# Performance work log

Hardware: AMD Instinct MI355X
Metric: run time of the kernel (lower is better)

The kernel has to match this reference:

```python
import jax, jax.numpy as jnp
import numpy as np

B, T, C, HS = 8, 4096, 1024, 128

def setup_inputs() -> dict:
    key = jax.random.key(0)
    kx, kq, kk, kv = jax.random.split(key, 4)
    x = jax.random.normal(kx, (B, T, C), dtype=jnp.float32)
    # Linear weights stored as [in, out] so projection is x @ W
    Wq = jax.random.normal(kq, (C, HS), dtype=jnp.float32) * (C ** -0.5)
    Wk = jax.random.normal(kk, (C, HS), dtype=jnp.float32) * (C ** -0.5)
    Wv = jax.random.normal(kv, (C, HS), dtype=jnp.float32) * (C ** -0.5)
    return {"x": x, "Wq": Wq, "Wk": Wk, "Wv": Wv}

def reference(x, Wq, Wk, Wv):
    # one head of causal self-attention (dropout=0.0 -> identity)
    q = x @ Wq  # [B,T,HS]
    k = x @ Wk
    v = x @ Wv
    scale = q.shape[-1] ** -0.5
    scores = jnp.einsum('bqd,bkd->bqk', q, k) * scale  # [B,T,T]
    t = q.shape[1]
    causal = jnp.tril(jnp.ones((t, t), dtype=bool))
    scores = jnp.where(causal, scores, jnp.finfo(scores.dtype).min)
    weights = jax.nn.softmax(scores, axis=-1)
    out = jnp.einsum('bqk,bkd->bqd', weights, v)  # [B,T,HS]
    return out
```

## Files before the change

kernel.cpp:

```cpp
#include <hip/hip_runtime.h>
#include <hip/hip_bf16.h>

#define TB 8
#define TT 4096
#define TC 1024
#define THS 128

typedef __bf16 bf16;
typedef __attribute__((ext_vector_type(8))) __bf16 bf16x8;
typedef __attribute__((ext_vector_type(2))) __bf16 bf16x2;
typedef __attribute__((ext_vector_type(4))) float f32x4;
typedef __attribute__((ext_vector_type(16))) float f32x16;

__device__ __forceinline__ unsigned pkbf(float a, float b) {
    bf16x2 t = { (bf16)a, (bf16)b };
    return __builtin_bit_cast(unsigned, t);
}

__device__ __forceinline__ void gload16(const void* g, void* l) {
    __builtin_amdgcn_global_load_lds(
        (const __attribute__((address_space(1))) void*)g,
        (__attribute__((address_space(3))) void*)l, 16, 0, 0);
}

__global__ __launch_bounds__(256) void wt_kernel(const float* __restrict__ Wq,
                                                 const float* __restrict__ Wk,
                                                 const float* __restrict__ Wv,
                                                 bf16* __restrict__ Wt) {
    __shared__ float tile[64][65];
    const int tid = threadIdx.x;
    const int idx = blockIdx.x;
    const int w = idx >> 5;
    const int kt = (idx & 31) >> 1, ntb = idx & 1;
    const int k0 = kt * 64, n0 = ntb * 64;
    const float* W = (w == 0) ? Wq : (w == 1) ? Wk : Wv;
    #pragma unroll
    for (int i = 0; i < 4; i++) {
        int r = (tid >> 4) + i * 16;
        int c4 = (tid & 15) * 4;
        float4 x4 = *reinterpret_cast<const float4*>(&W[(long)(k0 + r) * 128 + n0 + c4]);
        tile[r][c4 + 0] = x4.x; tile[r][c4 + 1] = x4.y;
        tile[r][c4 + 2] = x4.z; tile[r][c4 + 3] = x4.w;
    }
    __syncthreads();
    const int n = tid >> 2, kk = (tid & 3) * 16;
    bf16 o[16];
    #pragma unroll
    for (int j = 0; j < 16; j++) o[j] = (bf16)tile[kk + j][n];
    bf16* dst = &Wt[(long)((w << 7) + n0 + n) * 1024 + k0 + kk];
    *reinterpret_cast<bf16x8*>(dst)     = *reinterpret_cast<bf16x8*>(&o[0]);
    *reinterpret_cast<bf16x8*>(dst + 8) = *reinterpret_cast<bf16x8*>(&o[8]);
}

__global__ __launch_bounds__(256, 2) void qkv_kernel(const float* __restrict__ x,
                                                     const bf16* __restrict__ Wt,
                                                     bf16* __restrict__ Q,
                                                     bf16* __restrict__ K,
                                                     bf16* __restrict__ V) {
    __shared__ __align__(1024) char wsm[2][24576];
    __shared__ __align__(1024) char xsm[2][8192];
    const int tid = threadIdx.x;
    const int wave = tid >> 6, lane = tid & 63;
    const int lr = lane & 15, g = lane >> 4;
    const long row0 = (long)blockIdx.x * 64;

    long wOff[6]; int wLoff[6];
    #pragma unroll
    for (int i = 0; i < 6; i++) {
        int D = i * 4096 + wave * 1024 + lane * 16;
        int n = D >> 6, kb2 = D & 63;
        wOff[i] = (long)n * 2048 + (kb2 ^ ((n & 3) << 4));
        wLoff[i] = i * 4096 + wave * 1024;
    }
    long xOff[2]; int xLoff[2];
    #pragma unroll
    for (int i = 0; i < 2; i++) {
        int D = wave * 2048 + i * 1024 + lane * 16;
        int xr = D >> 7, xcb = D & 127;
        xOff[i] = (long)xr * 4096 + (xcb ^ ((xr & 7) << 4));
        xLoff[i] = wave * 2048 + i * 1024;
    }
    const char* xb = (const char*)x + row0 * 4096;
    const char* wb = (const char*)Wt;

    f32x4 acc[4][6] = {};

    {
        #pragma unroll
        for (int i = 0; i < 6; i++) gload16(wb + wOff[i], &wsm[0][0] + wLoff[i]);
        #pragma unroll
        for (int i = 0; i < 2; i++) gload16(xb + xOff[i], &xsm[0][0] + xLoff[i]);
    }
    asm volatile("s_waitcnt vmcnt(0)" ::: "memory");
    __builtin_amdgcn_s_barrier();

    const int asw = (lr & 7) << 4;
    const int bsw = (lr & 3) << 4;
    #pragma unroll 1
    for (int s = 0; s < 32; s++) {
        const int bi = s & 1;
        if (s + 1 < 32) {
            const char* wsrc = wb + (long)(s + 1) * 64;
            const char* xsrc = xb + (long)(s + 1) * 128;
            #pragma unroll
            for (int i = 0; i < 6; i++) gload16(wsrc + wOff[i], &wsm[bi ^ 1][0] + wLoff[i]);
            #pragma unroll
            for (int i = 0; i < 2; i++) gload16(xsrc + xOff[i], &xsm[bi ^ 1][0] + xLoff[i]);
        }
        const char* xp = &xsm[bi][0];
        const char* wp = &wsm[bi][0];
        bf16x8 a[4];
        #pragma unroll
        for (int ar = 0; ar < 4; ar++) {
            const int rbase = (ar * 16 + lr) * 128;
            f32x4 lo = *reinterpret_cast<const f32x4*>(xp + rbase + ((g * 32) ^ asw));
            f32x4 hi4 = *reinterpret_cast<const f32x4*>(xp + rbase + ((g * 32 + 16) ^ asw));
            uint4 u;
            u.x = pkbf(lo[0], lo[1]); u.y = pkbf(lo[2], lo[3]);
            u.z = pkbf(hi4[0], hi4[1]); u.w = pkbf(hi4[2], hi4[3]);
            a[ar] = __builtin_bit_cast(bf16x8, u);
        }
        #pragma unroll
        for (int nt = 0; nt < 6; nt++) {
            const int n = wave * 96 + nt * 16 + lr;
            bf16x8 bfr = *reinterpret_cast<const bf16x8*>(wp + n * 64 + ((g * 16) ^ bsw));
            #pragma unroll
            for (int ar = 0; ar < 4; ar++)
                acc[ar][nt] = __builtin_amdgcn_mfma_f32_16x16x32_bf16(a[ar], bfr, acc[ar][nt], 0, 0, 0);
        }
        asm volatile("s_waitcnt vmcnt(0)" ::: "memory");
        __builtin_amdgcn_s_barrier();
    }
    const float qscale = 0.08838834764831845f;
    bf16* outs[3] = {Q, K, V};
    #pragma unroll
    for (int nt = 0; nt < 6; nt++) {
        const int col = wave * 96 + nt * 16 + lr;
        const int w = col >> 7, d = col & 127;
        #pragma unroll
        for (int ar = 0; ar < 4; ar++)
            #pragma unroll
            for (int r = 0; r < 4; r++) {
                float val = acc[ar][nt][r];
                if (w == 0) val *= qscale;
                long row = row0 + ar * 16 + g * 4 + r;
                outs[w][row * 128 + d] = (bf16)val;
            }
    }
}

__global__ __launch_bounds__(256) void vtrans_kernel(const bf16* __restrict__ V,
                                                     bf16* __restrict__ Vtt) {
    __shared__ __align__(16) bf16 tile[64][136];
    const int tid = threadIdx.x;
    const int b = blockIdx.y;
    const int tt = blockIdx.x;
    const long ibase = ((long)b * TT + tt * 64) * 128;
    #pragma unroll
    for (int i = 0; i < 4; i++) {
        int slot = tid + 256 * i;
        int r = slot >> 4, c8 = (slot & 15) * 8;
        *reinterpret_cast<bf16x8*>(&tile[r][c8]) =
            *reinterpret_cast<const bf16x8*>(&V[ibase + r * 128 + c8]);
    }
    __syncthreads();
    #pragma unroll
    for (int i = 0; i < 4; i++) {
        int slot = tid + 256 * i;
        int d = slot >> 3, t8 = (slot & 7) * 8;
        bf16x8 v;
        #pragma unroll
        for (int j = 0; j < 8; j++) v[j] = tile[t8 + j][d];
        *reinterpret_cast<bf16x8*>(&Vtt[(((long)b * 64 + tt) * 128 + d) * 64 + t8]) = v;
    }
}

__global__ __launch_bounds__(512, 2) void attn_kernel(const bf16* __restrict__ Q,
                                                      const bf16* __restrict__ K,
                                                      const bf16* __restrict__ Vtt,
                                                      float* __restrict__ out) {
    __shared__ __align__(1024) char smem[131072];
    __shared__ float mlb[6 * 64];
    const int tid = threadIdx.x;
    const int wave = tid >> 6, lane = tid & 63;
    const int c = lane & 31, hi = lane >> 5;
    const int qs = wave >> 2, kvq = wave & 3;
    const int kswz = ((c & 7) << 4) ^ (((c >> 3) & 1) << 7);
    const int vswz = (c & 7) << 4;
    const int v = blockIdx.x >> 3, b = blockIdx.x & 7;
    const long base = (long)b * TT * 128;
    const char* Kb = (const char*)(K + base);
    const char* Vb = (const char*)Vtt + (long)b * (64 * 16384);

    int kOff[4], vOff[4], lOff[4];
    #pragma unroll
    for (int i = 0; i < 4; i++) {
        int D = wave * 4096 + i * 1024 + lane * 16;
        kOff[i] = (D & ~255) | ((D & 255) ^ (((D >> 8) & 7) << 4) ^ (((D >> 11) & 1) << 7));
        vOff[i] = (D & ~127) | ((D & 127) ^ (((D >> 7) & 7) << 4));
        lOff[i] = wave * 4096 + i * 1024;
    }

    #pragma unroll 1
    for (int ph = 0; ph < 2; ph++) {
        const int qt = ph ? 63 - v : v;
        const int nIt = (qt + 2) >> 1;
        const int q0w = qt * 64 + qs * 32;
        const int qa = q0w + c;

        bf16x8 qf[8];
        #pragma unroll
        for (int dw = 0; dw < 8; dw++)
            qf[dw] = *reinterpret_cast<const bf16x8*>(&Q[base + (long)qa * 128 + dw * 16 + hi * 8]);

        f32x16 O[4] = {};
        float m = -__builtin_inff(), l = 0.f;

        {
            #pragma unroll
            for (int i = 0; i < 4; i++) {
                gload16(Kb + kOff[i], smem + lOff[i]);
                gload16(Vb + vOff[i], smem + 65536 + lOff[i]);
            }
            if (nIt > 1) {
                #pragma unroll
                for (int i = 0; i < 4; i++) {
                    gload16(Kb + 32768 + kOff[i], smem + 32768 + lOff[i]);
                    gload16(Vb + 32768 + vOff[i], smem + 98304 + lOff[i]);
                }
            }
        }

        #pragma unroll 1
        for (int it = 0; it < nIt; it++) {
            const int bi = it & 1;
            char* kBuf = smem + bi * 32768;
            char* vBuf = smem + 65536 + bi * 32768;
            if (it + 1 < nIt) asm volatile("s_waitcnt vmcnt(8)" ::: "memory");
            else              asm volatile("s_waitcnt vmcnt(0)" ::: "memory");
            __builtin_amdgcn_s_barrier();

            const int kv0 = it * 128 + kvq * 32;
            if (kv0 <= q0w) {
                const char* kb = kBuf + kvq * 8192;
                const char* vb = vBuf + (kvq >> 1) * 16384;
                const int vcol0 = (kvq & 1) * 64;
                f32x16 S = {};
                __builtin_amdgcn_s_setprio(1);
                #pragma unroll
                for (int dw = 0; dw < 8; dw++) {
                    bf16x8 kf = *reinterpret_cast<const bf16x8*>(
                        kb + c * 256 + ((dw * 32 + hi * 16) ^ kswz));
                    S = __builtin_amdgcn_mfma_f32_32x32x16_bf16(kf, qf[dw], S, 0, 0, 0);
                }
                __builtin_amdgcn_s_setprio(0);
                if (kv0 == q0w) {
                    #pragma unroll
                    for (int i = 0; i < 16; i++) {
                        int kvr = kv0 + (i & 3) + 8 * (i >> 2) + 4 * hi;
                        if (kvr > qa) S[i] = -__builtin_inff();
                    }
                }
                float t8[8];
                #pragma unroll
                for (int i = 0; i < 8; i++) t8[i] = fmaxf(S[i], S[i + 8]);
                float t4a = fmaxf(t8[0], t8[4]), t4b = fmaxf(t8[1], t8[5]);
                float t4c = fmaxf(t8[2], t8[6]), t4d = fmaxf(t8[3], t8[7]);
                float pm = fmaxf(fmaxf(t4a, t4b), fmaxf(t4c, t4d));
                pm = fmaxf(pm, __shfl_xor(pm, 32, 64));
                if (!__all(pm - m <= 8.0f)) {
                    float mn = fmaxf(m, pm);
                    float fr = __expf(m - mn);
                    #pragma unroll
                    for (int dt = 0; dt < 4; dt++) O[dt] = O[dt] * fr;
                    l *= fr;
                    m = mn;
                }
                #pragma unroll
                for (int i = 0; i < 16; i++) S[i] = __expf(S[i] - m);
                float s8[8];
                #pragma unroll
                for (int i = 0; i < 8; i++) s8[i] = S[i] + S[i + 8];
                l += ((s8[0] + s8[4]) + (s8[1] + s8[5])) + ((s8[2] + s8[6]) + (s8[3] + s8[7]));

                bf16x8 pf[2];
                #pragma unroll
                for (int wl = 0; wl < 2; wl++) {
                    const int i0 = 8 * wl;
                    unsigned L0 = pkbf(S[i0 + 0], S[i0 + 1]);
                    unsigned L1 = pkbf(S[i0 + 2], S[i0 + 3]);
                    unsigned H0 = pkbf(S[i0 + 4], S[i0 + 5]);
                    unsigned H1 = pkbf(S[i0 + 6], S[i0 + 7]);
                    unsigned sel0 = hi ? L0 : H0;
                    unsigned sel1 = hi ? L1 : H1;
                    unsigned x0 = __shfl_xor((int)sel0, 32, 64);
                    unsigned x1 = __shfl_xor((int)sel1, 32, 64);
                    uint4 f;
                    f.x = hi ? x0 : L0;
                    f.y = hi ? x1 : L1;
                    f.z = hi ? H0 : x0;
                    f.w = hi ? H1 : x1;
                    pf[wl] = __builtin_bit_cast(bf16x8, f);
                }
                __builtin_amdgcn_s_setprio(1);
                #pragma unroll
                for (int wl = 0; wl < 2; wl++)
                    #pragma unroll
                    for (int dt = 0; dt < 4; dt++) {
                        bf16x8 vf = *reinterpret_cast<const bf16x8*>(
                            vb + (dt * 32 + c) * 128 + ((vcol0 + wl * 32 + hi * 16) ^ vswz));
                        O[dt] = __builtin_amdgcn_mfma_f32_32x32x16_bf16(vf, pf[wl], O[dt], 0, 0, 0);
                    }
                __builtin_amdgcn_s_setprio(0);
            }
            __builtin_amdgcn_s_barrier();
            if (it + 2 < nIt) {
                const char* Ks = Kb + (long)(it + 2) * 32768;
                const char* Vs = Vb + (long)(it + 2) * 32768;
                #pragma unroll
                for (int i = 0; i < 4; i++) {
                    gload16(Ks + kOff[i], kBuf + lOff[i]);
                    gload16(Vs + vOff[i], vBuf + lOff[i]);
                }
            }
        }

        l += __shfl_xor(l, 32, 64);

        if (kvq != 0) {
            const int sl = qs * 3 + (kvq - 1);
            char* om = smem + sl * 16384;
            #pragma unroll
            for (int dt = 0; dt < 4; dt++)
                #pragma unroll
                for (int g = 0; g < 4; g++) {
                    float4 w4 = { O[dt][4 * g + 0], O[dt][4 * g + 1],
                                  O[dt][4 * g + 2], O[dt][4 * g + 3] };
                    *reinterpret_cast<float4*>(
                        om + c * 512 + ((dt * 128 + g * 32 + hi * 16) ^ ((c & 7) << 4))) = w4;
                }
            if (hi == 0) { mlb[sl * 64 + c] = m; mlb[sl * 64 + 32 + c] = l; }
        }
        __syncthreads();
        if (kvq == 0) {
            float mq[3], lq[3];
            float mx = m;
            #pragma unroll
            for (int p = 0; p < 3; p++) {
                const int sl = qs * 3 + p;
                mq[p] = mlb[sl * 64 + c];
                lq[p] = mlb[sl * 64 + 32 + c];
                mx = fmaxf(mx, mq[p]);
            }
            float f0 = __expf(m - mx);
            float lt = l * f0;
            float fq[3];
            #pragma unroll
            for (int p = 0; p < 3; p++) { fq[p] = __expf(mq[p] - mx); lt += lq[p] * fq[p]; }
            float linv = 1.0f / lt;
            #pragma unroll
            for (int dt = 0; dt < 4; dt++)
                #pragma unroll
                for (int g = 0; g < 4; g++) {
                    float4 r;
                    r.x = O[dt][4 * g + 0] * f0;
                    r.y = O[dt][4 * g + 1] * f0;
                    r.z = O[dt][4 * g + 2] * f0;
                    r.w = O[dt][4 * g + 3] * f0;
                    #pragma unroll
                    for (int p = 0; p < 3; p++) {
                        const char* om = smem + (qs * 3 + p) * 16384;
                        float4 o1 = *reinterpret_cast<const float4*>(
                            om + c * 512 + ((dt * 128 + g * 32 + hi * 16) ^ ((c & 7) << 4)));
                        r.x += o1.x * fq[p]; r.y += o1.y * fq[p];
                        r.z += o1.z * fq[p]; r.w += o1.w * fq[p];
                    }
                    r.x *= linv; r.y *= linv; r.z *= linv; r.w *= linv;
                    *reinterpret_cast<float4*>(
                        &out[base + (long)qa * 128 + dt * 32 + 8 * g + 4 * hi]) = r;
                }
        }
        __syncthreads();
    }
}

extern "C" void kernel_launch(void* const* d_in, const int* in_sizes, int n_in,
                              void* d_out, int out_size, void* d_ws, size_t ws_size,
                              hipStream_t stream) {
    const float* x  = (const float*)d_in[0];
    const float* Wq = (const float*)d_in[1];
    const float* Wk = (const float*)d_in[2];
    const float* Wv = (const float*)d_in[3];
    float* out = (float*)d_out;
    bf16* Q   = (bf16*)d_ws;
    bf16* K   = Q   + (size_t)32768 * 128;
    bf16* V   = K   + (size_t)32768 * 128;
    bf16* Wt  = V   + (size_t)32768 * 128;
    bf16* Vtt = Wt  + (size_t)3 * 128 * 1024;
    wt_kernel<<<96, 256, 0, stream>>>(Wq, Wk, Wv, Wt);
    qkv_kernel<<<512, 256, 0, stream>>>(x, Wt, Q, K, V);
    vtrans_kernel<<<dim3(64, 8), 256, 0, stream>>>(V, Vtt);
    attn_kernel<<<256, 512, 0, stream>>>(Q, K, Vtt, out);
}
```

Baseline: 116.9 us.

## Retile QKV projection GEMM to 128-row blocks with deeper pipelined K steps

The QKV projection kernel now uses 512-thread blocks covering 128 rows, split into two row halves and four column groups, so each weight tile is reused by twice as many rows. The K step grows from 32 to 64, giving 16 iterations instead of 32. The x tiles are triple-staged through a two-buffer ring with partial vmcnt waits, so the next x load overlaps compute, and s_setprio is raised around the MFMA block. This is meant to cut weight-load traffic and per-step barrier overhead, at the cost of 112KB of LDS per block (one block per CU), half as many blocks, and a single-buffered weight tile that is reloaded after a barrier.

After: 118.4 us. About the same (+1.3%).

```diff
diff --git a/kernel.cpp b/kernel.cpp
--- a/kernel.cpp
+++ b/kernel.cpp
@@ -52,33 +52,33 @@
     *reinterpret_cast<bf16x8*>(dst + 8) = *reinterpret_cast<bf16x8*>(&o[8]);
 }
 
-__global__ __launch_bounds__(256, 2) void qkv_kernel(const float* __restrict__ x,
+__global__ __launch_bounds__(512, 2) void qkv_kernel(const float* __restrict__ x,
                                                      const bf16* __restrict__ Wt,
                                                      bf16* __restrict__ Q,
                                                      bf16* __restrict__ K,
                                                      bf16* __restrict__ V) {
-    __shared__ __align__(1024) char wsm[2][24576];
-    __shared__ __align__(1024) char xsm[2][8192];
+    __shared__ __align__(1024) char smem[114688];
     const int tid = threadIdx.x;
     const int wave = tid >> 6, lane = tid & 63;
     const int lr = lane & 15, g = lane >> 4;
-    const long row0 = (long)blockIdx.x * 64;
-
-    long wOff[6]; int wLoff[6];
+    const int qs = wave >> 2, ns = wave & 3;
+    const long row0 = (long)blockIdx.x * 128;
+
+    int xOff[4], xL[4];
+    #pragma unroll
+    for (int i = 0; i < 4; i++) {
+        int D = wave * 4096 + i * 1024 + lane * 16;
+        int r = D >> 8, c = D & 255;
+        xOff[i] = r * 4096 + (c ^ (((r & 7) << 4) ^ (((r >> 3) & 1) << 7)));
+        xL[i] = wave * 4096 + i * 1024;
+    }
+    int wOff[6], wL[6];
     #pragma unroll
     for (int i = 0; i < 6; i++) {
-        int D = i * 4096 + wave * 1024 + lane * 16;
-        int n = D >> 6, kb2 = D & 63;
-        wOff[i] = (long)n * 2048 + (kb2 ^ ((n & 3) << 4));
-        wLoff[i] = i * 4096 + wave * 1024;
-    }
-    long xOff[2]; int xLoff[2];
-    #pragma unroll
-    for (int i = 0; i < 2; i++) {
-        int D = wave * 2048 + i * 1024 + lane * 16;
-        int xr = D >> 7, xcb = D & 127;
-        xOff[i] = (long)xr * 4096 + (xcb ^ ((xr & 7) << 4));
-        xLoff[i] = wave * 2048 + i * 1024;
+        int D = wave * 6144 + i * 1024 + lane * 16;
+        int n = D >> 7, c = D & 127;
+        wOff[i] = n * 2048 + (c ^ ((n & 7) << 4));
+        wL[i] = wave * 6144 + i * 1024;
     }
     const char* xb = (const char*)x + row0 * 4096;
     const char* wb = (const char*)Wt;
@@ -87,55 +87,69 @@
 
     {
         #pragma unroll
-        for (int i = 0; i < 6; i++) gload16(wb + wOff[i], &wsm[0][0] + wLoff[i]);
-        #pragma unroll
-        for (int i = 0; i < 2; i++) gload16(xb + xOff[i], &xsm[0][0] + xLoff[i]);
-    }
-    asm volatile("s_waitcnt vmcnt(0)" ::: "memory");
-    __builtin_amdgcn_s_barrier();
-
-    const int asw = (lr & 7) << 4;
-    const int bsw = (lr & 3) << 4;
+        for (int i = 0; i < 4; i++) gload16(xb + xOff[i], smem + xL[i]);
+        #pragma unroll
+        for (int i = 0; i < 6; i++) gload16(wb + wOff[i], smem + 65536 + wL[i]);
+        #pragma unroll
+        for (int i = 0; i < 4; i++) gload16(xb + 256 + xOff[i], smem + 32768 + xL[i]);
+    }
+
     #pragma unroll 1
-    for (int s = 0; s < 32; s++) {
-        const int bi = s & 1;
-        if (s + 1 < 32) {
-            const char* wsrc = wb + (long)(s + 1) * 64;
-            const char* xsrc = xb + (long)(s + 1) * 128;
-            #pragma unroll
-            for (int i = 0; i < 6; i++) gload16(wsrc + wOff[i], &wsm[bi ^ 1][0] + wLoff[i]);
-            #pragma unroll
-            for (int i = 0; i < 2; i++) gload16(xsrc + xOff[i], &xsm[bi ^ 1][0] + xLoff[i]);
-        }
-        const char* xp = &xsm[bi][0];
-        const char* wp = &wsm[bi][0];
-        bf16x8 a[4];
+    for (int s = 0; s < 16; s++) {
+        if (s < 15) asm volatile("s_waitcnt vmcnt(4)" ::: "memory");
+        else        asm volatile("s_waitcnt vmcnt(0)" ::: "memory");
+        __builtin_amdgcn_s_barrier();
+
+        const char* xp = smem + (s & 1) * 32768;
+        const char* wp = smem + 65536;
+        bf16x8 a[4][2];
         #pragma unroll
         for (int ar = 0; ar < 4; ar++) {
-            const int rbase = (ar * 16 + lr) * 128;
-            f32x4 lo = *reinterpret_cast<const f32x4*>(xp + rbase + ((g * 32) ^ asw));
-            f32x4 hi4 = *reinterpret_cast<const f32x4*>(xp + rbase + ((g * 32 + 16) ^ asw));
-            uint4 u;
-            u.x = pkbf(lo[0], lo[1]); u.y = pkbf(lo[2], lo[3]);
-            u.z = pkbf(hi4[0], hi4[1]); u.w = pkbf(hi4[2], hi4[3]);
-            a[ar] = __builtin_bit_cast(bf16x8, u);
-        }
+            const int r = qs * 64 + ar * 16 + lr;
+            const int rs = ((r & 7) << 4) ^ (((r >> 3) & 1) << 7);
+            #pragma unroll
+            for (int ks = 0; ks < 2; ks++) {
+                f32x4 lo  = *reinterpret_cast<const f32x4*>(xp + r * 256 + ((ks * 128 + g * 32) ^ rs));
+                f32x4 hi4 = *reinterpret_cast<const f32x4*>(xp + r * 256 + ((ks * 128 + g * 32 + 16) ^ rs));
+                uint4 u;
+                u.x = pkbf(lo[0], lo[1]);  u.y = pkbf(lo[2], lo[3]);
+                u.z = pkbf(hi4[0], hi4[1]); u.w = pkbf(hi4[2], hi4[3]);
+                a[ar][ks] = __builtin_bit_cast(bf16x8, u);
+            }
+        }
+        __builtin_amdgcn_s_setprio(1);
         #pragma unroll
         for (int nt = 0; nt < 6; nt++) {
-            const int n = wave * 96 + nt * 16 + lr;
-            bf16x8 bfr = *reinterpret_cast<const bf16x8*>(wp + n * 64 + ((g * 16) ^ bsw));
-            #pragma unroll
-            for (int ar = 0; ar < 4; ar++)
-                acc[ar][nt] = __builtin_amdgcn_mfma_f32_16x16x32_bf16(a[ar], bfr, acc[ar][nt], 0, 0, 0);
-        }
-        asm volatile("s_waitcnt vmcnt(0)" ::: "memory");
+            const int n = ns * 96 + nt * 16 + lr;
+            const int nsw = (n & 7) << 4;
+            #pragma unroll
+            for (int ks = 0; ks < 2; ks++) {
+                bf16x8 bfr = *reinterpret_cast<const bf16x8*>(wp + n * 128 + ((ks * 64 + g * 16) ^ nsw));
+                #pragma unroll
+                for (int ar = 0; ar < 4; ar++)
+                    acc[ar][nt] = __builtin_amdgcn_mfma_f32_16x16x32_bf16(a[ar][ks], bfr, acc[ar][nt], 0, 0, 0);
+            }
+        }
+        __builtin_amdgcn_s_setprio(0);
         __builtin_amdgcn_s_barrier();
-    }
+
+        if (s + 1 < 16) {
+            #pragma unroll
+            for (int i = 0; i < 6; i++)
+                gload16(wb + (s + 1) * 128 + wOff[i], smem + 65536 + wL[i]);
+        }
+        if (s + 2 < 16) {
+            #pragma unroll
+            for (int i = 0; i < 4; i++)
+                gload16(xb + (s + 2) * 256 + xOff[i], smem + (s & 1) * 32768 + xL[i]);
+        }
+    }
+
     const float qscale = 0.08838834764831845f;
     bf16* outs[3] = {Q, K, V};
     #pragma unroll
     for (int nt = 0; nt < 6; nt++) {
-        const int col = wave * 96 + nt * 16 + lr;
+        const int col = ns * 96 + nt * 16 + lr;
         const int w = col >> 7, d = col & 127;
         #pragma unroll
         for (int ar = 0; ar < 4; ar++)
@@ -143,7 +157,7 @@
             for (int r = 0; r < 4; r++) {
                 float val = acc[ar][nt][r];
                 if (w == 0) val *= qscale;
-                long row = row0 + ar * 16 + g * 4 + r;
+                long row = row0 + qs * 64 + ar * 16 + g * 4 + r;
                 outs[w][row * 128 + d] = (bf16)val;
             }
     }
@@ -398,7 +412,7 @@
     bf16* Wt  = V   + (size_t)32768 * 128;
     bf16* Vtt = Wt  + (size_t)3 * 128 * 1024;
     wt_kernel<<<96, 256, 0, stream>>>(Wq, Wk, Wv, Wt);
-    qkv_kernel<<<512, 256, 0, stream>>>(x, Wt, Q, K, V);
+    qkv_kernel<<<256, 512, 0, stream>>>(x, Wt, Q, K, V);
     vtrans_kernel<<<dim3(64, 8), 256, 0, stream>>>(V, Vtt);
     attn_kernel<<<256, 512, 0, stream>>>(Q, K, Vtt, out);
 }
```
